# Performance work log

Measured on AMD Instinct MI355X. Metric: run time of the kernel, lower is better.

The kernel has to match this reference:

```python
import jax, jax.numpy as jnp
import numpy as np

NEG_POS_RATIO = 3
LOC_LOSS_ALPHA = 1.0
B, N, C = 64, 8732, 21  # batch, total prior boxes (SSD300), classes (VOC)


def setup_inputs() -> dict:
    key = jax.random.key(0)
    kd, km, kl, kpd, kpl = jax.random.split(key, 5)
    pos_mask = jax.random.bernoulli(km, 0.02, (B, N))
    actual_bbox_deltas = jax.random.normal(kd, (B, N, 4), dtype=jnp.float32) * pos_mask[..., None]
    cls = jax.random.randint(kl, (B, N), 0, C)
    actual_labels = jax.nn.one_hot(cls, C, dtype=jnp.float32)
    pred_bbox_deltas = jax.random.normal(kpd, (B, N, 4), dtype=jnp.float32)
    pred_labels = jax.random.normal(kpl, (B, N, C), dtype=jnp.float32)
    return {
        "actual_bbox_deltas": actual_bbox_deltas,
        "actual_labels": actual_labels,
        "pred_bbox_deltas": pred_bbox_deltas,
        "pred_labels": pred_labels,
    }


def reference(actual_bbox_deltas, actual_labels, pred_bbox_deltas, pred_labels):
    # positive boxes: any nonzero delta
    pos_cond = jnp.any(actual_bbox_deltas != 0, axis=2)          # [B, N] bool
    pos_count = jnp.sum(pos_cond, axis=1)                         # [B]
    neg_count = pos_count * NEG_POS_RATIO                         # [B]

    # CE from logits, used only to rank negatives for hard-negative mining
    ce_logits = -jnp.sum(actual_labels * jax.nn.log_softmax(pred_labels, axis=-1), axis=-1)  # [B, N]
    masked_loss = jnp.where(pos_cond, -jnp.inf, ce_logits)
    # rank[b, n] = position of box n in descending sort of masked_loss[b]
    order = jnp.argsort(-masked_loss, axis=1)
    rank = jnp.argsort(order, axis=1)
    neg_mask = rank < neg_count[:, None]                          # hardest negatives
    sel_mask = pos_cond | neg_mask                                # boxes entering conf loss

    total_pos = jnp.maximum(jnp.sum(pos_count), 1).astype(jnp.float32)

    # Huber (delta=1): TF Huber takes mean over last axis, then reduction='sum'
    d = pred_bbox_deltas - actual_bbox_deltas
    ad = jnp.abs(d)
    hub = jnp.where(ad <= 1.0, 0.5 * d * d, ad - 0.5)             # [B, N, 4]
    loc_loss = jnp.sum(jnp.mean(hub, axis=-1) * pos_cond) * LOC_LOSS_ALPHA

    # conf loss: TF CategoricalCrossentropy with from_logits=False (as in the original code,
    # applied to the raw pred_labels): normalize to sum 1, clip to epsilon, -sum(y*log p)
    eps = 1e-7
    p = pred_labels / jnp.sum(pred_labels, axis=-1, keepdims=True)
    p = jnp.clip(p, eps, 1.0 - eps)
    ce_probs = -jnp.sum(actual_labels * jnp.log(p), axis=-1)      # [B, N]
    conf_loss = jnp.sum(ce_probs * sel_mask)

    return loc_loss / total_pos, conf_loss / total_pos
```

## Files before the change

### kernel.cpp

```cpp
#include <hip/hip_runtime.h>
#include <math.h>

#define BB 64
#define NN 8732
#define NV4 (NN / 4)
#define CC 21
#define TB 256
#define GX 35

static __device__ __forceinline__ unsigned f2u(float f) {
  unsigned u = __float_as_uint(f);
  return (u & 0x80000000u) ? ~u : (u | 0x80000000u);
}

__global__ __launch_bounds__(256) void k1_map(
    const float* __restrict__ abd, const float* __restrict__ lbl,
    const float* __restrict__ pbd, const float* __restrict__ plog,
    unsigned* __restrict__ keys, float* __restrict__ cep,
    float* __restrict__ pl, float* __restrict__ pc, int* __restrict__ pcnt) {
  __shared__ float s_l[4], s_p[4];
  __shared__ int s_c[4];

  const int b = blockIdx.y;
  const int n = blockIdx.x * TB + threadIdx.x;
  const int tid = threadIdx.x;
  const bool valid = n < NN;
  float loc = 0.f, pconf = 0.f;
  int isPos = 0;
  if (valid) {
    const size_t idx = (size_t)b * NN + n;
    const float4 a = reinterpret_cast<const float4*>(abd)[idx];
    const float4 p = reinterpret_cast<const float4*>(pbd)[idx];
    isPos = (a.x != 0.f) || (a.y != 0.f) || (a.z != 0.f) || (a.w != 0.f);

    const float* pr = plog + idx * CC;
    const float* lr = lbl + idx * CC;
    float pv[CC];
    float m = -INFINITY, ssum = 0.f, tdot = 0.f;
#pragma unroll
    for (int j = 0; j < CC; ++j) {
      const float v = pr[j];
      pv[j] = v;
      m = fmaxf(m, v);
      ssum += v;
    }
    float es = 0.f;
#pragma unroll
    for (int j = 0; j < CC; ++j) {
      es += expf(pv[j] - m);
      tdot = fmaf(lr[j], pv[j], tdot);
    }
    const float pt = tdot / ssum;
    const float ptc = fminf(fmaxf(pt, 1e-7f), 1.0f - 1e-7f);
    const float cp = -logf(ptc);
    const float cel = (m + logf(es)) - tdot;
    keys[idx] = isPos ? 0u : f2u(cel);
    cep[idx] = cp;
    pconf = isPos ? cp : 0.f;
    const float dx = p.x - a.x, dy = p.y - a.y, dz = p.z - a.z, dw = p.w - a.w;
    const float axv = fabsf(dx), ayv = fabsf(dy), azv = fabsf(dz), awv = fabsf(dw);
    const float h = (axv <= 1.f ? 0.5f * dx * dx : axv - 0.5f)
                  + (ayv <= 1.f ? 0.5f * dy * dy : ayv - 0.5f)
                  + (azv <= 1.f ? 0.5f * dz * dz : azv - 0.5f)
                  + (awv <= 1.f ? 0.5f * dw * dw : awv - 0.5f);
    loc = isPos ? h * 0.25f : 0.f;
  }
  float lvv = loc, pcf = pconf;
  int pctr = isPos;
  for (int off = 32; off > 0; off >>= 1) {
    lvv += __shfl_down(lvv, off, 64);
    pcf += __shfl_down(pcf, off, 64);
    pctr += __shfl_down(pctr, off, 64);
  }
  const int lane = tid & 63, wv = tid >> 6;
  if (lane == 0) { s_l[wv] = lvv; s_p[wv] = pcf; s_c[wv] = pctr; }
  __syncthreads();
  if (tid == 0) {
    const int bi = b * GX + blockIdx.x;
    pl[bi] = s_l[0] + s_l[1] + s_l[2] + s_l[3];
    pc[bi] = s_p[0] + s_p[1] + s_p[2] + s_p[3];
    pcnt[bi] = s_c[0] + s_c[1] + s_c[2] + s_c[3];
  }
}

#define K2T 1024
#define K2W 16

__global__ __launch_bounds__(K2T) void k2_select(
    const unsigned* __restrict__ keys, const float* __restrict__ cep,
    const float* __restrict__ pl, const float* __restrict__ pc,
    const int* __restrict__ pcnt,
    double* __restrict__ row_loc, double* __restrict__ row_conf,
    int* __restrict__ row_pos) {
  __shared__ unsigned hist[2048];
  __shared__ unsigned wsum[K2W];
  __shared__ unsigned bc[2];
  __shared__ unsigned wtot[K2W];
  __shared__ double s_d[K2W];
  __shared__ double s_rl, s_rc;
  __shared__ int s_pos;
  const int b = blockIdx.x;
  const int tid = threadIdx.x;
  const int lane = tid & 63, wv = tid >> 6;

  if (wv == 0) {
    float a = 0.f, c = 0.f;
    int p = 0;
    if (lane < GX) {
      a = pl[b * GX + lane];
      c = pc[b * GX + lane];
      p = pcnt[b * GX + lane];
    }
    for (int off = 32; off > 0; off >>= 1) {
      a += __shfl_down(a, off, 64);
      c += __shfl_down(c, off, 64);
      p += __shfl_down(p, off, 64);
    }
    if (lane == 0) { s_rl = (double)a; s_rc = (double)c; s_pos = p; }
  }
  __syncthreads();
  const int pos = s_pos;
  unsigned k = (unsigned)(pos * 3);
  const unsigned negs = (unsigned)(NN - pos);
  if (k > negs) k = negs;

  double neg_total = 0.0;
  if (k > 0) {
    const unsigned* rk = keys + (size_t)b * NN;
    const uint4* rk4 = reinterpret_cast<const uint4*>(rk);
    unsigned want = k;
    unsigned prefix = 0;
    for (int pass = 0; pass < 3; ++pass) {
      const int nb = (pass == 2) ? 1024 : 2048;
      const int shift = (pass == 0) ? 21 : (pass == 1) ? 10 : 0;
      for (int i = tid; i < nb; i += K2T) hist[i] = 0;
      __syncthreads();
      if (pass == 0) {
        for (int t = tid; t < NV4; t += K2T) {
          uint4 v = rk4[t];
          atomicAdd(&hist[v.x >> 21], 1u);
          atomicAdd(&hist[v.y >> 21], 1u);
          atomicAdd(&hist[v.z >> 21], 1u);
          atomicAdd(&hist[v.w >> 21], 1u);
        }
      } else {
        const unsigned pshift = (pass == 1) ? 21u : 10u;
        const unsigned msk = (unsigned)(nb - 1);
        for (int t = tid; t < NV4; t += K2T) {
          uint4 v = rk4[t];
          if ((v.x >> pshift) == prefix) atomicAdd(&hist[(v.x >> shift) & msk], 1u);
          if ((v.y >> pshift) == prefix) atomicAdd(&hist[(v.y >> shift) & msk], 1u);
          if ((v.z >> pshift) == prefix) atomicAdd(&hist[(v.z >> shift) & msk], 1u);
          if ((v.w >> pshift) == prefix) atomicAdd(&hist[(v.w >> shift) & msk], 1u);
        }
      }
      __syncthreads();
      const int PR = nb / K2T;
      unsigned v0, v1 = 0, ls;
      if (PR == 2) {
        v0 = hist[nb - 1 - (tid * 2)];
        v1 = hist[nb - 1 - (tid * 2 + 1)];
        ls = v0 + v1;
      } else {
        v0 = hist[nb - 1 - tid];
        ls = v0;
      }
      unsigned x = ls;
#pragma unroll
      for (int off = 1; off < 64; off <<= 1) {
        unsigned y = __shfl_up(x, off, 64);
        if (lane >= off) x += y;
      }
      if (lane == 63) wsum[wv] = x;
      __syncthreads();
      if (wv == 0 && lane < K2W) {
        unsigned wx = wsum[lane];
#pragma unroll
        for (int off = 1; off < K2W; off <<= 1) {
          unsigned wy = __shfl_up(wx, off, K2W);
          if ((lane & (K2W - 1)) >= off) wx += wy;
        }
        wsum[lane] = wx;
      }
      __syncthreads();
      const unsigned woff = (wv == 0) ? 0u : wsum[wv - 1];
      const unsigned pinc = woff + x;
      if (PR == 2) {
        const unsigned p0 = pinc - ls + v0;
        const unsigned p1 = pinc;
        if (v0 > 0 && p0 >= want && p0 - v0 < want) { bc[0] = (unsigned)(nb - 1 - tid * 2); bc[1] = want - (p0 - v0); }
        if (v1 > 0 && p1 >= want && p1 - v1 < want) { bc[0] = (unsigned)(nb - 1 - (tid * 2 + 1)); bc[1] = want - (p1 - v1); }
      } else {
        if (v0 > 0 && pinc >= want && pinc - v0 < want) { bc[0] = (unsigned)(nb - 1 - tid); bc[1] = want - (pinc - v0); }
      }
      __syncthreads();
      const unsigned d = bc[0];
      want = bc[1];
      prefix = (pass == 0) ? d : ((prefix << ((pass == 1) ? 11 : 10)) | d);
      __syncthreads();
    }
    const unsigned tau = prefix;
    const unsigned neq = want;

    const float* rc = cep + (size_t)b * NN;
    double mysum = 0.0;
    unsigned bbase = 0;
    for (int start = 0; start < NN; start += K2T) {
      const int i = start + tid;
      const unsigned key = (i < NN) ? rk[i] : 0u;
      const bool gt = (i < NN) && (key > tau);
      const bool eq = (i < NN) && (key == tau);
      if (gt) mysum += (double)rc[i];
      const unsigned long long mb = __ballot(eq);
      if (lane == 0) wtot[wv] = (unsigned)__popcll(mb);
      __syncthreads();
      unsigned wpref = 0, tot = 0;
#pragma unroll
      for (int w = 0; w < K2W; ++w) {
        const unsigned c = wtot[w];
        wpref += (w < wv) ? c : 0u;
        tot += c;
      }
      if (eq) {
        const unsigned lanepref = (unsigned)__popcll(mb & ((1ull << lane) - 1ull));
        if (bbase + wpref + lanepref < neq) mysum += (double)rc[i];
      }
      bbase += tot;
      __syncthreads();
    }
    for (int off = 32; off > 0; off >>= 1) mysum += __shfl_down(mysum, off, 64);
    if (lane == 0) s_d[wv] = mysum;
    __syncthreads();
    if (tid == 0) {
#pragma unroll
      for (int w = 0; w < K2W; ++w) neg_total += s_d[w];
    }
  }
  if (tid == 0) {
    row_loc[b] = s_rl;
    row_conf[b] = s_rc + neg_total;
    row_pos[b] = pos;
  }
}

__global__ void k3_final(const double* __restrict__ row_loc,
                         const double* __restrict__ row_conf,
                         const int* __restrict__ row_pos,
                         float* __restrict__ out) {
  const int lane = threadIdx.x;
  double l = row_loc[lane], c = row_conf[lane];
  int p = row_pos[lane];
  for (int off = 32; off > 0; off >>= 1) {
    l += __shfl_down(l, off, 64);
    c += __shfl_down(c, off, 64);
    p += __shfl_down(p, off, 64);
  }
  if (lane == 0) {
    const double tot = (p > 0) ? (double)p : 1.0;
    out[0] = (float)(l / tot);
    out[1] = (float)(c / tot);
  }
}

extern "C" void kernel_launch(void* const* d_in, const int* in_sizes, int n_in,
                              void* d_out, int out_size, void* d_ws, size_t ws_size,
                              hipStream_t stream) {
  const float* abd = (const float*)d_in[0];
  const float* lbl = (const float*)d_in[1];
  const float* pbd = (const float*)d_in[2];
  const float* plog = (const float*)d_in[3];

  char* ws = (char*)d_ws;
  float* pl = (float*)(ws + 0);
  float* pc = (float*)(ws + 8960);
  int* pcnt = (int*)(ws + 17920);
  double* row_loc = (double*)(ws + 26880);
  double* row_conf = (double*)(ws + 27392);
  int* row_pos = (int*)(ws + 27904);
  unsigned* keys = (unsigned*)(ws + 28160);
  float* cep = (float*)(ws + 28160 + (size_t)BB * NN * sizeof(unsigned));

  dim3 g1(GX, BB);
  k1_map<<<g1, TB, 0, stream>>>(abd, lbl, pbd, plog, keys, cep, pl, pc, pcnt);
  k2_select<<<BB, K2T, 0, stream>>>(keys, cep, pl, pc, pcnt, row_loc, row_conf, row_pos);
  k3_final<<<1, 64, 0, stream>>>(row_loc, row_conf, row_pos, (float*)d_out);
}
```

Measured before the change: 40.98 us.

## Process four boxes per thread with 16-byte vector loads in map kernel

The map kernel now assigns four consecutive boxes to each thread and reads their 84 logits and 84 labels as 21 float4 vectors each, splitting the values across four per-box softmax accumulators. Keys and CE values are written as a single 16-byte store. Blocks shrink to a single 64-thread wavefront, which removes the shared-memory reduction and the __syncthreads. The aim is fewer, wider memory transactions on the heavy label and logit streams. The cost is high register pressure from holding 84 floats per thread, and fewer resident waves to hide memory latency.

```diff
diff --git a/kernel.cpp b/kernel.cpp
--- a/kernel.cpp
+++ b/kernel.cpp
@@ -5,81 +5,111 @@
 #define NN 8732
 #define NV4 (NN / 4)
 #define CC 21
-#define TB 256
 #define GX 35
+
+typedef float vf4 __attribute__((ext_vector_type(4)));
 
 static __device__ __forceinline__ unsigned f2u(float f) {
   unsigned u = __float_as_uint(f);
   return (u & 0x80000000u) ? ~u : (u | 0x80000000u);
 }
 
-__global__ __launch_bounds__(256) void k1_map(
+__global__ __launch_bounds__(64, 2) void k1_map(
     const float* __restrict__ abd, const float* __restrict__ lbl,
     const float* __restrict__ pbd, const float* __restrict__ plog,
     unsigned* __restrict__ keys, float* __restrict__ cep,
     float* __restrict__ pl, float* __restrict__ pc, int* __restrict__ pcnt) {
-  __shared__ float s_l[4], s_p[4];
-  __shared__ int s_c[4];
-
   const int b = blockIdx.y;
-  const int n = blockIdx.x * TB + threadIdx.x;
-  const int tid = threadIdx.x;
-  const bool valid = n < NN;
+  const int q = blockIdx.x * 64 + threadIdx.x;
+  const bool valid = q < NV4;
+
   float loc = 0.f, pconf = 0.f;
-  int isPos = 0;
+  int cnt = 0;
   if (valid) {
-    const size_t idx = (size_t)b * NN + n;
-    const float4 a = reinterpret_cast<const float4*>(abd)[idx];
-    const float4 p = reinterpret_cast<const float4*>(pbd)[idx];
-    isPos = (a.x != 0.f) || (a.y != 0.f) || (a.z != 0.f) || (a.w != 0.f);
-
-    const float* pr = plog + idx * CC;
-    const float* lr = lbl + idx * CC;
-    float pv[CC];
-    float m = -INFINITY, ssum = 0.f, tdot = 0.f;
-#pragma unroll
-    for (int j = 0; j < CC; ++j) {
-      const float v = pr[j];
-      pv[j] = v;
-      m = fmaxf(m, v);
-      ssum += v;
-    }
-    float es = 0.f;
-#pragma unroll
-    for (int j = 0; j < CC; ++j) {
-      es += expf(pv[j] - m);
-      tdot = fmaf(lr[j], pv[j], tdot);
-    }
-    const float pt = tdot / ssum;
-    const float ptc = fminf(fmaxf(pt, 1e-7f), 1.0f - 1e-7f);
-    const float cp = -logf(ptc);
-    const float cel = (m + logf(es)) - tdot;
-    keys[idx] = isPos ? 0u : f2u(cel);
-    cep[idx] = cp;
-    pconf = isPos ? cp : 0.f;
-    const float dx = p.x - a.x, dy = p.y - a.y, dz = p.z - a.z, dw = p.w - a.w;
-    const float axv = fabsf(dx), ayv = fabsf(dy), azv = fabsf(dz), awv = fabsf(dw);
-    const float h = (axv <= 1.f ? 0.5f * dx * dx : axv - 0.5f)
-                  + (ayv <= 1.f ? 0.5f * dy * dy : ayv - 0.5f)
-                  + (azv <= 1.f ? 0.5f * dz * dz : azv - 0.5f)
-                  + (awv <= 1.f ? 0.5f * dw * dw : awv - 0.5f);
-    loc = isPos ? h * 0.25f : 0.f;
+    const size_t boxbase = (size_t)b * NN + (size_t)q * 4;
+    const vf4* Pr = reinterpret_cast<const vf4*>(plog + boxbase * CC);
+    const vf4* Lr = reinterpret_cast<const vf4*>(lbl + boxbase * CC);
+
+    vf4 P[21];
+    float m0 = -INFINITY, m1 = -INFINITY, m2 = -INFINITY, m3 = -INFINITY;
+    float s0 = 0.f, s1 = 0.f, s2 = 0.f, s3 = 0.f;
+    float t0 = 0.f, t1 = 0.f, t2 = 0.f, t3 = 0.f;
+#pragma unroll
+    for (int k = 0; k < 21; ++k) {
+      P[k] = Pr[k];
+      const vf4 Lk = Lr[k];
+#pragma unroll
+      for (int j = 0; j < 4; ++j) {
+        const int p = 4 * k + j;
+        const int r = p / 21;
+        const float v = P[k][j];
+        const float lv = Lk[j];
+        if (r == 0) { m0 = fmaxf(m0, v); s0 += v; t0 = fmaf(lv, v, t0); }
+        else if (r == 1) { m1 = fmaxf(m1, v); s1 += v; t1 = fmaf(lv, v, t1); }
+        else if (r == 2) { m2 = fmaxf(m2, v); s2 += v; t2 = fmaf(lv, v, t2); }
+        else { m3 = fmaxf(m3, v); s3 += v; t3 = fmaf(lv, v, t3); }
+      }
+    }
+    float e0 = 0.f, e1 = 0.f, e2 = 0.f, e3 = 0.f;
+#pragma unroll
+    for (int k = 0; k < 21; ++k) {
+#pragma unroll
+      for (int j = 0; j < 4; ++j) {
+        const int p = 4 * k + j;
+        const int r = p / 21;
+        const float v = P[k][j];
+        if (r == 0) e0 += expf(v - m0);
+        else if (r == 1) e1 += expf(v - m1);
+        else if (r == 2) e2 += expf(v - m2);
+        else e3 += expf(v - m3);
+      }
+    }
+    const float M[4] = {m0, m1, m2, m3};
+    const float S[4] = {s0, s1, s2, s3};
+    const float T[4] = {t0, t1, t2, t3};
+    const float E[4] = {e0, e1, e2, e3};
+
+    const float4* A4 = reinterpret_cast<const float4*>(abd) + boxbase;
+    const float4* B4 = reinterpret_cast<const float4*>(pbd) + boxbase;
+    unsigned kv[4];
+    float cv[4];
+#pragma unroll
+    for (int r = 0; r < 4; ++r) {
+      const float4 a = A4[r];
+      const float4 p = B4[r];
+      const int isPos =
+          (a.x != 0.f) || (a.y != 0.f) || (a.z != 0.f) || (a.w != 0.f);
+      const float pt = T[r] / S[r];
+      const float ptc = fminf(fmaxf(pt, 1e-7f), 1.0f - 1e-7f);
+      const float cp = -logf(ptc);
+      const float cel = (M[r] + logf(E[r])) - T[r];
+      kv[r] = isPos ? 0u : f2u(cel);
+      cv[r] = cp;
+      const float dx = p.x - a.x, dy = p.y - a.y, dz = p.z - a.z, dw = p.w - a.w;
+      const float ax = fabsf(dx), ay = fabsf(dy), az = fabsf(dz), aw = fabsf(dw);
+      const float h = (ax <= 1.f ? 0.5f * dx * dx : ax - 0.5f)
+                    + (ay <= 1.f ? 0.5f * dy * dy : ay - 0.5f)
+                    + (az <= 1.f ? 0.5f * dz * dz : az - 0.5f)
+                    + (aw <= 1.f ? 0.5f * dw * dw : aw - 0.5f);
+      if (isPos) { loc += h * 0.25f; pconf += cp; cnt += 1; }
+    }
+    *reinterpret_cast<uint4*>(keys + boxbase) =
+        make_uint4(kv[0], kv[1], kv[2], kv[3]);
+    *reinterpret_cast<float4*>(cep + boxbase) =
+        make_float4(cv[0], cv[1], cv[2], cv[3]);
   }
   float lvv = loc, pcf = pconf;
-  int pctr = isPos;
+  int pctr = cnt;
   for (int off = 32; off > 0; off >>= 1) {
     lvv += __shfl_down(lvv, off, 64);
     pcf += __shfl_down(pcf, off, 64);
     pctr += __shfl_down(pctr, off, 64);
   }
-  const int lane = tid & 63, wv = tid >> 6;
-  if (lane == 0) { s_l[wv] = lvv; s_p[wv] = pcf; s_c[wv] = pctr; }
-  __syncthreads();
-  if (tid == 0) {
+  if (threadIdx.x == 0) {
     const int bi = b * GX + blockIdx.x;
-    pl[bi] = s_l[0] + s_l[1] + s_l[2] + s_l[3];
-    pc[bi] = s_p[0] + s_p[1] + s_p[2] + s_p[3];
-    pcnt[bi] = s_c[0] + s_c[1] + s_c[2] + s_c[3];
+    pl[bi] = lvv;
+    pc[bi] = pcf;
+    pcnt[bi] = pctr;
   }
 }
 
@@ -281,7 +311,7 @@
   float* cep = (float*)(ws + 28160 + (size_t)BB * NN * sizeof(unsigned));
 
   dim3 g1(GX, BB);
-  k1_map<<<g1, TB, 0, stream>>>(abd, lbl, pbd, plog, keys, cep, pl, pc, pcnt);
+  k1_map<<<g1, 64, 0, stream>>>(abd, lbl, pbd, plog, keys, cep, pl, pc, pcnt);
   k2_select<<<BB, K2T, 0, stream>>>(keys, cep, pl, pc, pcnt, row_loc, row_conf, row_pos);
   k3_final<<<1, 64, 0, stream>>>(row_loc, row_conf, row_pos, (float*)d_out);
 }
```

Result: slower. 56.56 us (+38.0%).
